# Kernel tuning notes

Measured on AMD Instinct MI355X. Metric: run time of the kernel, lower is better.

Reference implementation:

```python
import jax, jax.numpy as jnp
import numpy as np


def setup_inputs() -> dict:
    key = jax.random.key(0)
    k1, k2 = jax.random.split(key)
    pred_m = jax.random.normal(k1, (64, 1, 512, 512), dtype=jnp.float32)
    # boxes: (x, y, s_x, s_y) per (batch, frame, target); values in [0, 256)
    multi_targets = jax.random.randint(k2, (64, 5, 32, 4), 0, 256, dtype=jnp.int32)
    return {"pred_m": pred_m, "multi_targets": multi_targets}


def _paint_heatmap(multi_targets, B, H, W, dtype):
    """Vectorized replacement for the triple-nested box-fill loop.

    Uses a 2D difference-array scatter + double cumsum: each box adds
    +1/-1 at its four corners; after prefix sums, count>0 marks painted
    pixels (original sets them to 255 regardless of overlap).
    """
    gt = multi_targets.reshape(B, -1, 4)  # [B, N, 4], N = n_frames*n_targets
    x, y, sx, sy = gt[..., 0], gt[..., 1], gt[..., 2], gt[..., 3]
    # python slicing clamps the end of the slice at H/W
    x1 = jnp.minimum(x, H)
    y1 = jnp.minimum(y, W)
    x2 = jnp.minimum(x + sx, H)
    y2 = jnp.minimum(y + sy, W)
    b_idx = jnp.broadcast_to(jnp.arange(B)[:, None], x.shape)
    diff = jnp.zeros((B, H + 1, W + 1), jnp.int32)
    diff = diff.at[b_idx, x1, y1].add(1)
    diff = diff.at[b_idx, x1, y2].add(-1)
    diff = diff.at[b_idx, x2, y1].add(-1)
    diff = diff.at[b_idx, x2, y2].add(1)
    count = jnp.cumsum(jnp.cumsum(diff, axis=1), axis=2)[:, :H, :W]
    return (count > 0).astype(dtype) * jnp.asarray(255.0, dtype)


def reference(pred_m, multi_targets):
    B, _, H, W = pred_m.shape
    heatmap = _paint_heatmap(multi_targets, B, H, W, pred_m.dtype)  # [B, H, W]
    target = heatmap[:, None]            # [B, 1, H, W]
    pred = jax.nn.sigmoid(pred_m)        # [B, 1, H, W]
    smooth = jnp.asarray(1.0, pred_m.dtype)
    intersection = jnp.sum(pred * target, axis=(1, 2, 3))
    pred_sum = jnp.sum(pred, axis=(1, 2, 3))
    target_sum = jnp.sum(target, axis=(1, 2, 3))
    loss = (intersection + smooth) / (pred_sum + target_sum - intersection + smooth)
    return 1.0 - jnp.mean(loss)
```

## Files before the change

kernel.cpp:

```cpp
#include <hip/hip_runtime.h>
#include <math.h>

#define SLICES 32
#define ROWS_PER_SLICE 16
#define NBOXES 160
#define THREADS 256

static __device__ __forceinline__ float fast_sigmoid(float x) {
    return __builtin_amdgcn_rcpf(1.0f + __expf(-x));
}

__global__ __launch_bounds__(THREADS) void paint_reduce_kernel(
    const float* __restrict__ pred, const int* __restrict__ targets,
    float* __restrict__ partials)
{
    __shared__ int s_x1[NBOXES], s_x2[NBOXES];
    __shared__ unsigned s_y1[NBOXES], s_y2[NBOXES];
    __shared__ int s_wcnt[4];
    __shared__ unsigned s_mask[ROWS_PER_SLICE * 16];
    __shared__ float s_red[4 * 3];

    const int t = threadIdx.x;
    const int slice = blockIdx.x;
    const int b = blockIdx.y;
    const int r0 = slice * ROWS_PER_SLICE;
    const int lane = t & 63, wave = t >> 6;

    int4 g = make_int4(0, 0, 0, 0);
    if (t < NBOXES) g = ((const int4*)targets)[(size_t)b * NBOXES + t];

    const float4* p4 = (const float4*)pred;
    const int col4 = t & 127;
    const int rb = t >> 7;
    const size_t g0 = (size_t)b * 65536 + (size_t)r0 * 128 + col4;
    float4 v0 = p4[g0 + (size_t)(rb + 0) * 128];
    float4 v1 = p4[g0 + (size_t)(rb + 2) * 128];
    float4 v2 = p4[g0 + (size_t)(rb + 4) * 128];
    float4 v3 = p4[g0 + (size_t)(rb + 6) * 128];
    __builtin_amdgcn_sched_barrier(0);

    bool keep = false;
    int cx1 = 0, cx2 = 0;
    unsigned cy1 = 0, cy2 = 0;
    if (t < NBOXES) {
        int x1 = min(g.x, 512), y1 = min(g.y, 512);
        int x2 = min(g.x + g.z, 512), y2 = min(g.y + g.w, 512);
        cx1 = max(x1, r0); cx2 = min(x2, r0 + ROWS_PER_SLICE);
        cy1 = (unsigned)y1; cy2 = (unsigned)y2;
        keep = (cx2 > cx1) && (y2 > y1);
    }
    const unsigned long long bal = __ballot(keep);
    if (lane == 0) s_wcnt[wave] = (int)__popcll(bal);
    __syncthreads();
    int wbase_cnt = 0;
    for (int w = 0; w < wave; ++w) wbase_cnt += s_wcnt[w];
    const int nb = s_wcnt[0] + s_wcnt[1] + s_wcnt[2] + s_wcnt[3];
    if (keep) {
        const int idx = wbase_cnt + (int)__popcll(bal & ((1ull << lane) - 1ull));
        s_x1[idx] = cx1; s_x2[idx] = cx2; s_y1[idx] = cy1; s_y2[idx] = cy2;
    }
    __syncthreads();

    {
        const int row_l = t >> 4;
        const int w = t & 15;
        const int r = r0 + row_l;
        const unsigned wb = (unsigned)w * 32u;
        unsigned m = 0;
        for (int k = 0; k < nb; ++k) {
            if (r >= s_x1[k] && r < s_x2[k]) {
                unsigned lo = s_y1[k], hi = s_y2[k];
                lo = lo > wb ? lo : wb;
                hi = hi < wb + 32u ? hi : wb + 32u;
                if (hi > lo) {
                    unsigned n = hi - lo;
                    unsigned bits = (n >= 32u) ? 0xFFFFFFFFu : ((1u << n) - 1u);
                    m |= bits << (lo - wb);
                }
            }
        }
        s_mask[t] = m;
    }
    __syncthreads();

    const int widx = col4 >> 3;
    const unsigned bb = (unsigned)(col4 & 7) * 4u;
    unsigned n0 = (s_mask[(rb +  0) * 16 + widx] >> bb) & 0xFu;
    unsigned n1 = (s_mask[(rb +  2) * 16 + widx] >> bb) & 0xFu;
    unsigned n2 = (s_mask[(rb +  4) * 16 + widx] >> bb) & 0xFu;
    unsigned n3 = (s_mask[(rb +  6) * 16 + widx] >> bb) & 0xFu;

    float4 v4 = p4[g0 + (size_t)(rb +  8) * 128];
    float4 v5 = p4[g0 + (size_t)(rb + 10) * 128];
    float4 v6 = p4[g0 + (size_t)(rb + 12) * 128];
    float4 v7 = p4[g0 + (size_t)(rb + 14) * 128];

    float psum = 0.0f, isum = 0.0f;
    int cnt = 0;
#define ACC(V, N)                                                       \
    {                                                                   \
        float s0 = fast_sigmoid((V).x);                                 \
        float s1 = fast_sigmoid((V).y);                                 \
        float s2 = fast_sigmoid((V).z);                                 \
        float s3 = fast_sigmoid((V).w);                                 \
        psum += (s0 + s1) + (s2 + s3);                                  \
        cnt += __popc(N);                                               \
        isum += (((N) & 1u) ? s0 : 0.0f) + (((N) & 2u) ? s1 : 0.0f)     \
              + (((N) & 4u) ? s2 : 0.0f) + (((N) & 8u) ? s3 : 0.0f);    \
    }
    ACC(v0, n0) ACC(v1, n1) ACC(v2, n2) ACC(v3, n3)

    unsigned n4 = (s_mask[(rb +  8) * 16 + widx] >> bb) & 0xFu;
    unsigned n5 = (s_mask[(rb + 10) * 16 + widx] >> bb) & 0xFu;
    unsigned n6 = (s_mask[(rb + 12) * 16 + widx] >> bb) & 0xFu;
    unsigned n7 = (s_mask[(rb + 14) * 16 + widx] >> bb) & 0xFu;
    ACC(v4, n4) ACC(v5, n5) ACC(v6, n6) ACC(v7, n7)
#undef ACC
    float csum = (float)cnt;

    for (int off = 32; off > 0; off >>= 1) {
        psum += __shfl_down(psum, off);
        isum += __shfl_down(isum, off);
        csum += __shfl_down(csum, off);
    }
    if (lane == 0) {
        s_red[wave * 3 + 0] = psum;
        s_red[wave * 3 + 1] = isum;
        s_red[wave * 3 + 2] = csum;
    }
    __syncthreads();
    if (t == 0) {
        float P = 0, I = 0, C = 0;
        for (int w = 0; w < 4; ++w) {
            P += s_red[w * 3 + 0];
            I += s_red[w * 3 + 1];
            C += s_red[w * 3 + 2];
        }
        float* o = partials + ((size_t)b * SLICES + slice) * 3;
        o[0] = P; o[1] = I; o[2] = C;
    }
}

__global__ __launch_bounds__(64) void final_kernel(
    const float* __restrict__ partials, float* __restrict__ out)
{
    const int b = threadIdx.x;
    double P = 0, I = 0, C = 0;
    for (int s = 0; s < SLICES; ++s) {
        const float* p = partials + ((size_t)b * SLICES + s) * 3;
        P += (double)p[0]; I += (double)p[1]; C += (double)p[2];
    }
    const double inter = 255.0 * I;
    const double tsum  = 255.0 * C;
    double loss = (inter + 1.0) / (P + tsum - inter + 1.0);
    for (int off = 32; off > 0; off >>= 1) loss += __shfl_down(loss, off);
    if (b == 0) out[0] = (float)(1.0 - loss / 64.0);
}

extern "C" void kernel_launch(void* const* d_in, const int* in_sizes, int n_in,
                              void* d_out, int out_size, void* d_ws, size_t ws_size,
                              hipStream_t stream) {
    const float* pred    = (const float*)d_in[0];
    const int*   targets = (const int*)d_in[1];
    float* out = (float*)d_out;
    float* partials = (float*)d_ws;

    dim3 grid(SLICES, 64);
    paint_reduce_kernel<<<grid, THREADS, 0, stream>>>(pred, targets, partials);
    final_kernel<<<1, 64, 0, stream>>>(partials, out);
}
```

Measured before the change: 110.1 us.

## Replace shared-memory box compaction with per-wave ballot and readlane scanning

Each wave now loads all 160 boxes itself, clips them to the slice, and builds ballot masks. It then walks only the surviving boxes, fetching their coordinates by readlane from packed registers. This drops two __syncthreads barriers and the shared-memory box arrays, and the mask loop becomes branch-free. Launch bounds also request 8 blocks per CU. The cost is that every wave repeats the box loads and clipping, and the loop is serialized per box via scalar readlane.

```diff
diff --git a/kernel.cpp b/kernel.cpp
--- a/kernel.cpp
+++ b/kernel.cpp
@@ -10,13 +10,10 @@
     return __builtin_amdgcn_rcpf(1.0f + __expf(-x));
 }
 
-__global__ __launch_bounds__(THREADS) void paint_reduce_kernel(
+__global__ __launch_bounds__(THREADS, 8) void paint_reduce_kernel(
     const float* __restrict__ pred, const int* __restrict__ targets,
     float* __restrict__ partials)
 {
-    __shared__ int s_x1[NBOXES], s_x2[NBOXES];
-    __shared__ unsigned s_y1[NBOXES], s_y2[NBOXES];
-    __shared__ int s_wcnt[4];
     __shared__ unsigned s_mask[ROWS_PER_SLICE * 16];
     __shared__ float s_red[4 * 3];
 
@@ -26,61 +23,61 @@
     const int r0 = slice * ROWS_PER_SLICE;
     const int lane = t & 63, wave = t >> 6;
 
-    int4 g = make_int4(0, 0, 0, 0);
-    if (t < NBOXES) g = ((const int4*)targets)[(size_t)b * NBOXES + t];
+    const int4* tg = (const int4*)targets + (size_t)b * NBOXES;
+    int4 gb0 = tg[lane];
+    int4 gb1 = tg[64 + lane];
+    int4 gb2 = (lane < 32) ? tg[128 + lane] : make_int4(0, 0, 0, 0);
+
+    unsigned px0, py0, px1, py1, px2, py2;
+    auto clip = [&](int4 g, unsigned& px, unsigned& py) -> bool {
+        int x1 = min(g.x, 512), y1 = min(g.y, 512);
+        int x2 = min(g.x + g.z, 512), y2 = min(g.y + g.w, 512);
+        int cx1 = max(x1, r0), cx2 = min(x2, r0 + ROWS_PER_SLICE);
+        px = (unsigned)cx1 | ((unsigned)cx2 << 16);
+        py = (unsigned)y1 | ((unsigned)y2 << 16);
+        return (cx2 > cx1) && (y2 > y1);
+    };
+    bool k0 = clip(gb0, px0, py0);
+    bool k1 = clip(gb1, px1, py1);
+    bool k2 = clip(gb2, px2, py2) && (lane < 32);
+    unsigned long long m0 = __ballot(k0);
+    unsigned long long m1 = __ballot(k1);
+    unsigned long long m2 = __ballot(k2);
 
     const float4* p4 = (const float4*)pred;
     const int col4 = t & 127;
     const int rb = t >> 7;
-    const size_t g0 = (size_t)b * 65536 + (size_t)r0 * 128 + col4;
-    float4 v0 = p4[g0 + (size_t)(rb + 0) * 128];
-    float4 v1 = p4[g0 + (size_t)(rb + 2) * 128];
-    float4 v2 = p4[g0 + (size_t)(rb + 4) * 128];
-    float4 v3 = p4[g0 + (size_t)(rb + 6) * 128];
+    const size_t gbase = (size_t)b * 65536 + (size_t)r0 * 128 + col4;
+    float4 v0 = p4[gbase + (size_t)(rb + 0) * 128];
+    float4 v1 = p4[gbase + (size_t)(rb + 2) * 128];
+    float4 v2 = p4[gbase + (size_t)(rb + 4) * 128];
+    float4 v3 = p4[gbase + (size_t)(rb + 6) * 128];
     __builtin_amdgcn_sched_barrier(0);
 
-    bool keep = false;
-    int cx1 = 0, cx2 = 0;
-    unsigned cy1 = 0, cy2 = 0;
-    if (t < NBOXES) {
-        int x1 = min(g.x, 512), y1 = min(g.y, 512);
-        int x2 = min(g.x + g.z, 512), y2 = min(g.y + g.w, 512);
-        cx1 = max(x1, r0); cx2 = min(x2, r0 + ROWS_PER_SLICE);
-        cy1 = (unsigned)y1; cy2 = (unsigned)y2;
-        keep = (cx2 > cx1) && (y2 > y1);
-    }
-    const unsigned long long bal = __ballot(keep);
-    if (lane == 0) s_wcnt[wave] = (int)__popcll(bal);
-    __syncthreads();
-    int wbase_cnt = 0;
-    for (int w = 0; w < wave; ++w) wbase_cnt += s_wcnt[w];
-    const int nb = s_wcnt[0] + s_wcnt[1] + s_wcnt[2] + s_wcnt[3];
-    if (keep) {
-        const int idx = wbase_cnt + (int)__popcll(bal & ((1ull << lane) - 1ull));
-        s_x1[idx] = cx1; s_x2[idx] = cx2; s_y1[idx] = cy1; s_y2[idx] = cy2;
-    }
-    __syncthreads();
-
-    {
-        const int row_l = t >> 4;
-        const int w = t & 15;
-        const int r = r0 + row_l;
-        const unsigned wb = (unsigned)w * 32u;
-        unsigned m = 0;
-        for (int k = 0; k < nb; ++k) {
-            if (r >= s_x1[k] && r < s_x2[k]) {
-                unsigned lo = s_y1[k], hi = s_y2[k];
-                lo = lo > wb ? lo : wb;
-                hi = hi < wb + 32u ? hi : wb + 32u;
-                if (hi > lo) {
-                    unsigned n = hi - lo;
-                    unsigned bits = (n >= 32u) ? 0xFFFFFFFFu : ((1u << n) - 1u);
-                    m |= bits << (lo - wb);
-                }
-            }
+    const int r = r0 + (t >> 4);
+    const unsigned wb = (unsigned)(t & 15) * 32u;
+    unsigned m = 0;
+    auto scan = [&](unsigned long long mk, unsigned px, unsigned py) {
+        while (mk) {
+            int k = (int)__builtin_ctzll(mk);
+            mk &= mk - 1;
+            unsigned rx = (unsigned)__builtin_amdgcn_readlane((int)px, k);
+            unsigned ry = (unsigned)__builtin_amdgcn_readlane((int)py, k);
+            int x1 = (int)(rx & 0xffffu), x2 = (int)(rx >> 16);
+            unsigned y1 = ry & 0xffffu, y2 = ry >> 16;
+            bool in_row = (r >= x1) && (r < x2);
+            unsigned lo = y1 > wb ? y1 : wb;
+            unsigned hi = y2 < wb + 32u ? y2 : wb + 32u;
+            int nn = (int)hi - (int)lo;
+            unsigned bits = 0xFFFFFFFFu >> ((32 - nn) & 31);
+            unsigned contrib = bits << ((lo - wb) & 31u);
+            m |= (in_row && nn > 0) ? contrib : 0u;
         }
-        s_mask[t] = m;
-    }
+    };
+    scan(m0, px0, py0);
+    scan(m1, px1, py1);
+    scan(m2, px2, py2);
+    s_mask[t] = m;
     __syncthreads();
 
     const int widx = col4 >> 3;
@@ -90,10 +87,10 @@
     unsigned n2 = (s_mask[(rb +  4) * 16 + widx] >> bb) & 0xFu;
     unsigned n3 = (s_mask[(rb +  6) * 16 + widx] >> bb) & 0xFu;
 
-    float4 v4 = p4[g0 + (size_t)(rb +  8) * 128];
-    float4 v5 = p4[g0 + (size_t)(rb + 10) * 128];
-    float4 v6 = p4[g0 + (size_t)(rb + 12) * 128];
-    float4 v7 = p4[g0 + (size_t)(rb + 14) * 128];
+    float4 v4 = p4[gbase + (size_t)(rb +  8) * 128];
+    float4 v5 = p4[gbase + (size_t)(rb + 10) * 128];
+    float4 v6 = p4[gbase + (size_t)(rb + 12) * 128];
+    float4 v7 = p4[gbase + (size_t)(rb + 14) * 128];
 
     float psum = 0.0f, isum = 0.0f;
     int cnt = 0;
```

Result: faster. 106.7 us (-3.1%).
